# Performance work log

Measured on AMD Instinct MI355X. Metric: run time of the kernel, lower is better.

## Reference

```python
import jax, jax.numpy as jnp
import numpy as np

B, H, W, DIM = 16, 28, 28, 256
HEADS, K = 8, 7
HD = DIM // HEADS
MLP = int(DIM * 4.0)
EPS = 1e-5


def setup_inputs() -> dict:
    key = jax.random.key(0)
    ks = jax.random.split(key, 8)
    s = 0.02
    return {
        "x": jax.random.normal(ks[0], (B, H, W, DIM), jnp.float32),
        "norm1_w": jnp.ones((DIM,), jnp.float32),
        "norm1_b": jnp.zeros((DIM,), jnp.float32),
        "qkv_w": jax.random.normal(ks[1], (3 * DIM, DIM), jnp.float32) * s,
        "qkv_b": jnp.zeros((3 * DIM,), jnp.float32),
        "rpb": jax.random.normal(ks[2], (HEADS, 2 * K - 1, 2 * K - 1), jnp.float32) * s,
        "proj_w": jax.random.normal(ks[3], (DIM, DIM), jnp.float32) * s,
        "proj_b": jnp.zeros((DIM,), jnp.float32),
        "norm2_w": jnp.ones((DIM,), jnp.float32),
        "norm2_b": jnp.zeros((DIM,), jnp.float32),
        "fc1_w": jax.random.normal(ks[4], (MLP, DIM), jnp.float32) * s,
        "fc1_b": jnp.zeros((MLP,), jnp.float32),
        "fc2_w": jax.random.normal(ks[5], (DIM, MLP), jnp.float32) * s,
        "fc2_b": jnp.zeros((DIM,), jnp.float32),
    }


def _ln(x, w, b):
    m = jnp.mean(x, axis=-1, keepdims=True)
    v = jnp.var(x, axis=-1, keepdims=True)  # biased, as torch LayerNorm
    return (x - m) * jax.lax.rsqrt(v + EPS) * w + b


def _window_idx(n):
    # NATTEN border handling: window shifts so every query has exactly K neighbors
    start = jnp.clip(jnp.arange(n) - K // 2, 0, n - K)  # [n]
    idx = start[:, None] + jnp.arange(K)                # [n, K] absolute neighbor index
    rel = idx - jnp.arange(n)[:, None] + (K - 1)        # [n, K] rpb index in [0, 2K-2]
    return idx, rel


def _neighborhood_attn(x, qkv_w, qkv_b, rpb, proj_w, proj_b):
    b, h, w, c = x.shape
    qkv = (x @ qkv_w.T + qkv_b).reshape(b, h, w, 3, HEADS, HD)
    q, k, v = qkv[:, :, :, 0], qkv[:, :, :, 1], qkv[:, :, :, 2]  # [b,h,w,heads,hd]
    q = q * (HD ** -0.5)
    idx_h, rel_h = _window_idx(h)
    idx_w, rel_w = _window_idx(w)
    # gather K/V neighborhoods: [b,h,K,w,K,heads,hd]
    kwin = k[:, idx_h][:, :, :, idx_w]
    vwin = v[:, idx_h][:, :, :, idx_w]
    # logits per query (i,j) over its KxK window
    attn = jnp.einsum('bijhd,biajchd->bhijac', q, kwin)  # [b,heads,h,w,K,K]
    bias = rpb[:, rel_h]                 # [heads,h,K,2K-1]
    bias = bias[:, :, :, rel_w]          # [heads,h,K,w,K]
    bias = bias.transpose(0, 1, 3, 2, 4) # [heads,h,w,K,K]
    attn = attn + bias[None]
    attn = jax.nn.softmax(attn.reshape(b, HEADS, h, w, K * K), axis=-1)
    attn = attn.reshape(b, HEADS, h, w, K, K)
    out = jnp.einsum('bhijac,biajchd->bijhd', attn, vwin).reshape(b, h, w, c)
    return out @ proj_w.T + proj_b


def reference(x, norm1_w, norm1_b, qkv_w, qkv_b, rpb, proj_w, proj_b,
              norm2_w, norm2_b, fc1_w, fc1_b, fc2_w, fc2_b):
    shortcut = x
    x = _ln(x, norm1_w, norm1_b)
    x = shortcut + _neighborhood_attn(x, qkv_w, qkv_b, rpb, proj_w, proj_b)
    h = _ln(x, norm2_w, norm2_b) @ fc1_w.T + fc1_b
    h = jax.nn.gelu(h, approximate=False)  # torch nn.GELU default (erf)
    return x + (h @ fc2_w.T + fc2_b)
```

## Files before the change

kernel.cpp:

```cpp
#include <hip/hip_runtime.h>
#include <hip/hip_bf16.h>
#include <math.h>

#define DIM   256
#define HEADS 8
#define HD    32
#define KW    7
#define HH    28
#define WW    28
#define BBATCH 16
#define NTOK  (BBATCH*HH*WW)
#define MLPD  1024
#define EPSLN 1e-5f
#define QSCALE 0.17677669529663687f

#define AS1 __attribute__((address_space(1)))
#define AS3 __attribute__((address_space(3)))

typedef __attribute__((ext_vector_type(8))) short short8;
typedef __attribute__((ext_vector_type(4))) float f32x4;
typedef unsigned short us;

__device__ __forceinline__ float b2f(us u) {
  union { float f; unsigned u; } x; x.u = ((unsigned)u) << 16; return x.f;
}
__device__ __forceinline__ us f2b(float f) {
  union { float f; unsigned u; } x; x.f = f;
  unsigned lsb = (x.u >> 16) & 1;
  x.u += 0x7fffu + lsb;
  return (us)(x.u >> 16);
}
__device__ __forceinline__ bool probe_f32(const us* p) { return p[0] == 0; }

__device__ __forceinline__ void gll16(const us* g, us* l) {
  __builtin_amdgcn_global_load_lds((const AS1 unsigned*)(const void*)g,
                                   (AS3 unsigned*)(void*)l, 16, 0, 0);
}

__device__ __forceinline__ float gelu_f(float x) {
  const float y = 0.7978845608028654f * x * (1.0f + 0.044715f * x * x);
  const float u = __expf(2.0f * y);
  const float th = 1.0f - 2.0f / (u + 1.0f);
  return 0.5f * x * (1.0f + th);
}

__global__ __launch_bounds__(256) void pre_kernel(const void* s0, const void* s1,
                                                  const void* s2, const void* s3,
                                                  us* d0, us* d1, us* d2, us* d3,
                                                  const void* p0, const void* p1, const void* p2,
                                                  const void* p3, const void* p4, const void* p5,
                                                  const void* p6, const void* p7, const void* p8,
                                                  float* __restrict__ pack,
                                                  const void* __restrict__ x,
                                                  us* __restrict__ xn1,
                                                  us* __restrict__ bias_t,
                                                  const us* __restrict__ probe)
{
  const bool isf32 = probe_f32(probe);
  const int blk = blockIdx.x;
  const int t = threadIdx.x;
  if (blk < 768) {
    const int gi = (blk * 256 + t) * 4;
    const void* src; us* dst; int loc; bool qs = false;
    if (gi < 196608)      { src = s0; dst = d0; loc = gi; qs = (loc < 65536); }
    else if (gi < 262144) { src = s1; dst = d1; loc = gi - 196608; }
    else if (gi < 524288) { src = s2; dst = d2; loc = gi - 262144; }
    else                  { src = s3; dst = d3; loc = gi - 524288; }
    float v[4];
    if (isf32) {
      const float4 f = *(const float4*)((const float*)src + loc);
      v[0] = f.x; v[1] = f.y; v[2] = f.z; v[3] = f.w;
    } else {
      ushort4 u = *(const ushort4*)((const us*)src + loc);
      v[0] = b2f(u.x); v[1] = b2f(u.y); v[2] = b2f(u.z); v[3] = b2f(u.w);
    }
    const float sc = qs ? QSCALE : 1.0f;
    ushort4 o;
    o.x = f2b(v[0] * sc); o.y = f2b(v[1] * sc); o.z = f2b(v[2] * sc); o.w = f2b(v[3] * sc);
    *(ushort4*)(dst + loc) = o;
  } else if (blk < 777) {
    const int seg = blk - 768;
    const void* srcs[9] = {p0, p1, p2, p3, p4, p5, p6, p7, p8};
    const int offs[9] = {0, 256, 512, 1280, 1536, 1792, 2048, 3072, 3328};
    const int lens[9] = {256, 256, 768, 256, 256, 256, 1024, 256, 1352};
    const void* s = srcs[seg];
    const int off = offs[seg], len = lens[seg];
    for (int i = t; i < len; i += 256) {
      float v = isf32 ? ((const float*)s)[i] : b2f(((const us*)s)[i]);
      if (seg == 2 && i < 256) v *= QSCALE;
      pack[off + i] = v;
    }
  } else if (blk < 3913) {
    const int wave = t >> 6, lane = t & 63;
    const int tok = (blk - 777) * 4 + wave;
    const int c0 = lane * 4;
    float v[4];
    if (isf32) {
      const float4 f = *(const float4*)((const float*)x + (size_t)tok * DIM + c0);
      v[0] = f.x; v[1] = f.y; v[2] = f.z; v[3] = f.w;
    } else {
      ushort4 u = *(const ushort4*)((const us*)x + (size_t)tok * DIM + c0);
      v[0] = b2f(u.x); v[1] = b2f(u.y); v[2] = b2f(u.z); v[3] = b2f(u.w);
    }
    float s  = v[0] + v[1] + v[2] + v[3];
    float s2 = v[0]*v[0] + v[1]*v[1] + v[2]*v[2] + v[3]*v[3];
    #pragma unroll
    for (int m = 32; m; m >>= 1) { s += __shfl_xor(s, m); s2 += __shfl_xor(s2, m); }
    const float mean = s * (1.0f / DIM);
    const float var  = s2 * (1.0f / DIM) - mean * mean;
    const float rstd = rsqrtf(var + EPSLN);
    float wv[4], bv[4];
    if (isf32) {
      const float4 a = *(const float4*)((const float*)p0 + c0);
      const float4 c = *(const float4*)((const float*)p1 + c0);
      wv[0]=a.x; wv[1]=a.y; wv[2]=a.z; wv[3]=a.w;
      bv[0]=c.x; bv[1]=c.y; bv[2]=c.z; bv[3]=c.w;
    } else {
      ushort4 a = *(const ushort4*)((const us*)p0 + c0);
      ushort4 c = *(const ushort4*)((const us*)p1 + c0);
      wv[0]=b2f(a.x); wv[1]=b2f(a.y); wv[2]=b2f(a.z); wv[3]=b2f(a.w);
      bv[0]=b2f(c.x); bv[1]=b2f(c.y); bv[2]=b2f(c.z); bv[3]=b2f(c.w);
    }
    ushort4 o;
    o.x = f2b((v[0] - mean) * rstd * wv[0] + bv[0]);
    o.y = f2b((v[1] - mean) * rstd * wv[1] + bv[1]);
    o.z = f2b((v[2] - mean) * rstd * wv[2] + bv[2]);
    o.w = f2b((v[3] - mean) * rstd * wv[3] + bv[3]);
    *(ushort4*)(xn1 + (size_t)tok * DIM + c0) = o;
  } else {
    const int ph = blk - 3913;
    const int p  = ph >> 3, h = ph & 7;
    const int i0 = 2 * p;
    const int si0 = min(max(i0 - 3, 0), 21);
    us* bt = bias_t + (size_t)ph * (224 * 64);
    for (int e = 0; e < 56; ++e) {
      const int idx = e * 256 + t;
      const int kv = idx >> 6;
      const int q  = idx & 63;
      const int isub = q >> 5;
      const int cq = q & 31;
      const int iq = i0 + isub;
      const int siq = min(max(iq - 3, 0), 21);
      const int sj  = min(max(cq - 3, 0), 21);
      const int rr  = (kv * 2341) >> 16;
      const int ar  = si0 + rr;
      const int ck  = kv - rr * 28;
      const int dr = ar - siq, dc = ck - sj;
      const bool valid = (cq < 28) && (dr >= 0) && (dr < 7) && (dc >= 0) && (dc < 7);
      float ev = 0.f;
      if (valid) {
        const int ridx = h * 169 + (ar - iq + 6) * 13 + (ck - cq + 6);
        const float bvv = isf32 ? ((const float*)p8)[ridx] : b2f(((const us*)p8)[ridx]);
        ev = __expf(bvv);
      }
      bt[idx] = f2b(ev);
    }
  }
}

__global__ __launch_bounds__(256) void ln_kernel(const us* __restrict__ in,
                                                 const float* __restrict__ w,
                                                 const float* __restrict__ b,
                                                 us* __restrict__ out)
{
  const int t = threadIdx.x;
  const int wave = t >> 6, lane = t & 63;
  const int tok = blockIdx.x * 4 + wave;
  const int c0 = lane * 4;
  ushort4 u = *(const ushort4*)(in + (size_t)tok * DIM + c0);
  float v[4] = {b2f(u.x), b2f(u.y), b2f(u.z), b2f(u.w)};
  float s  = v[0] + v[1] + v[2] + v[3];
  float s2 = v[0]*v[0] + v[1]*v[1] + v[2]*v[2] + v[3]*v[3];
  #pragma unroll
  for (int m = 32; m; m >>= 1) { s += __shfl_xor(s, m); s2 += __shfl_xor(s2, m); }
  const float mean = s * (1.0f / DIM);
  const float var  = s2 * (1.0f / DIM) - mean * mean;
  const float rstd = rsqrtf(var + EPSLN);
  const float4 wv = *(const float4*)(w + c0);
  const float4 bv = *(const float4*)(b + c0);
  ushort4 o;
  o.x = f2b((v[0] - mean) * rstd * wv.x + bv.x);
  o.y = f2b((v[1] - mean) * rstd * wv.y + bv.y);
  o.z = f2b((v[2] - mean) * rstd * wv.z + bv.z);
  o.w = f2b((v[3] - mean) * rstd * wv.w + bv.w);
  *(ushort4*)(out + (size_t)tok * DIM + c0) = o;
}

template<int BM, int BN, int BK, int MODE>
__global__ __launch_bounds__(256) void gemm_kernel(const us* __restrict__ A,
                                                   const us* __restrict__ W,
                                                   const float* __restrict__ bias,
                                                   const void* __restrict__ resid,
                                                   void* __restrict__ out,
                                                   int N, int K,
                                                   const us* __restrict__ probe)
{
  constexpr int MF = BM / 32;
  constexpr int NF = BN / 32;
  constexpr int CPR = BK / 8;
  constexpr int ACH = BM * CPR;
  constexpr int BCH = BN * CPR;
  constexpr int ASZ = BM * BK;
  constexpr int BSZ = BN * BK;
  constexpr int TILEB = 2 * (ASZ + BSZ) * 2;
  constexpr int CSB = (MODE == 3) ? BM * BN * 4 : BM * BN * 2;
  constexpr int SMB = TILEB > CSB ? TILEB : CSB;
  __shared__ char smem[SMB];
  us* Asb = (us*)smem;
  us* Bsb = (us*)smem + 2 * ASZ;

  const int t = threadIdx.x;
  const int wave = t >> 6, lane = t & 63;
  const int wm = wave >> 1, wn = wave & 1;
  const int m0 = blockIdx.x * BM;
  const int n0 = blockIdx.y * BN;
  const int lm = lane & 15;
  const int g  = lane >> 4;

  const int NS = K / BK;

  #define STAGE(buf, kk)                                                         \
    {                                                                            \
      _Pragma("unroll")                                                          \
      for (int i = 0; i < ACH / 256; ++i) {                                      \
        const int slot = i * 256 + t;                                            \
        const int gc = slot ^ ((slot >> 3) & 7);                                 \
        gll16(A + (size_t)(m0 + gc / CPR) * K + (kk) + (gc % CPR) * 8,           \
              &Asb[(buf) * ASZ + slot * 8]);                                     \
      }                                                                          \
      _Pragma("unroll")                                                          \
      for (int i = 0; i < BCH / 256; ++i) {                                      \
        const int slot = i * 256 + t;                                            \
        const int gc = slot ^ ((slot >> 3) & 7);                                 \
        gll16(W + (size_t)(n0 + gc / CPR) * K + (kk) + (gc % CPR) * 8,           \
              &Bsb[(buf) * BSZ + slot * 8]);                                     \
      }                                                                          \
    }

  STAGE(0, 0);

  f32x4 acc[MF][NF] = {};
  int cur = 0;
  for (int s = 0; s < NS; ++s) {
    __syncthreads();
    if (s + 1 < NS) STAGE(cur ^ 1, (s + 1) * BK);
    #pragma unroll
    for (int kh = 0; kh < BK / 32; ++kh) {
      short8 a[MF], b[NF];
      #pragma unroll
      for (int mf = 0; mf < MF; ++mf) {
        const int row = wm * (BM / 2) + mf * 16 + lm;
        const int c = row * CPR + kh * 4 + g;
        const int sl = c ^ ((c >> 3) & 7);
        a[mf] = *(const short8*)(const void*)&Asb[cur * ASZ + sl * 8];
      }
      #pragma unroll
      for (int nf = 0; nf < NF; ++nf) {
        const int row = wn * (BN / 2) + nf * 16 + lm;
        const int c = row * CPR + kh * 4 + g;
        const int sl = c ^ ((c >> 3) & 7);
        b[nf] = *(const short8*)(const void*)&Bsb[cur * BSZ + sl * 8];
      }
      #pragma unroll
      for (int mf = 0; mf < MF; ++mf) {
        #pragma unroll
        for (int nf = 0; nf < NF; ++nf)
          acc[mf][nf] = __builtin_amdgcn_mfma_f32_16x16x32_bf16(a[mf], b[nf], acc[mf][nf], 0, 0, 0);
      }
    }
    cur ^= 1;
  }
  #undef STAGE

  const bool isf32 = (MODE == 1 || MODE == 3) ? probe_f32(probe) : false;
  const int col = lm;
  const int rb  = g * 4;
  __syncthreads();

  if (MODE == 3 && isf32) {
    float* Cf = (float*)smem;
    #pragma unroll
    for (int mf = 0; mf < MF; ++mf) {
      #pragma unroll
      for (int nf = 0; nf < NF; ++nf) {
        const int n_loc = wn * (BN / 2) + nf * 16 + col;
        const float bv = bias[n0 + n_loc];
        #pragma unroll
        for (int j = 0; j < 4; ++j) {
          const int m_loc = wm * (BM / 2) + mf * 16 + rb + j;
          const size_t off = (size_t)(m0 + m_loc) * N + (n0 + n_loc);
          float v = acc[mf][nf][j] + bv + b2f(((const us*)resid)[off]);
          Cf[m_loc * BN + (n_loc ^ ((m_loc & 7) << 3))] = v;
        }
      }
    }
    __syncthreads();
    constexpr int CH = BM * BN / 4;
    #pragma unroll
    for (int it = 0; it < CH / 256; ++it) {
      const int id = it * 256 + t;
      const int m = id / (BN / 4), c = id % (BN / 4);
      const float4 val = *(const float4*)&Cf[m * BN + ((c ^ ((m & 7) << 1)) * 4)];
      *(float4*)((float*)out + (size_t)(m0 + m) * N + n0 + c * 4) = val;
    }
  } else {
    us* Cs = (us*)smem;
    #pragma unroll
    for (int mf = 0; mf < MF; ++mf) {
      #pragma unroll
      for (int nf = 0; nf < NF; ++nf) {
        const int n_loc = wn * (BN / 2) + nf * 16 + col;
        const float bv = bias[n0 + n_loc];
        #pragma unroll
        for (int j = 0; j < 4; ++j) {
          const int m_loc = wm * (BM / 2) + mf * 16 + rb + j;
          const size_t off = (size_t)(m0 + m_loc) * N + (n0 + n_loc);
          float v = acc[mf][nf][j] + bv;
          if (MODE == 1) v += isf32 ? ((const float*)resid)[off] : b2f(((const us*)resid)[off]);
          else if (MODE == 2) v = gelu_f(v);
          else if (MODE == 3) v += b2f(((const us*)resid)[off]);
          Cs[m_loc * BN + (n_loc ^ ((m_loc & 7) << 3))] = f2b(v);
        }
      }
    }
    __syncthreads();
    constexpr int CH = BM * BN / 8;
    #pragma unroll
    for (int it = 0; it < CH / 256; ++it) {
      const int id = it * 256 + t;
      const int m = id / (BN / 8), c = id % (BN / 8);
      const uint4 val = *(const uint4*)&Cs[m * BN + (c ^ (m & 7)) * 8];
      *(uint4*)((us*)out + (size_t)(m0 + m) * N + n0 + c * 8) = val;
    }
  }
}

__global__ __launch_bounds__(256) void attn_kernel(const us* __restrict__ qkv,
                                                   const us* __restrict__ bias_t,
                                                   us* __restrict__ out)
{
  __shared__ us KP_lds[64 * 232];
  __shared__ us Vt_lds[32 * 232];

  const int raw = blockIdx.x;
  const int bid = (raw & 7) * 224 + (raw >> 3);
  const int b  = bid & 15;
  const int ph = bid >> 4;
  const int p  = ph >> 3;
  const int h  = ph & 7;
  const int i0 = 2 * p;
  const int t = threadIdx.x;
  const int wave = t >> 6, lane = t & 63;
  const int lm = lane & 15, g = lane >> 4;
  const int kb = g * 8;
  const int si0 = min(max(i0 - 3, 0), 21);
  const int si1 = min(max(i0 - 2, 0), 21);
  const int nch = (si1 + 7 - si0) * 112;

  const us* kg = qkv + ((size_t)(b * 784 + si0 * 28)) * 768 + 256 + h * 32;
  const us* vg = kg + 256;

  const int c0 = t, c1 = 256 + t, c2 = 512 + t, c3 = 768 + t;
  const bool has3 = c3 < nch;
  uint4 v0 = *(const uint4*)(const void*)(vg + (size_t)(c0 >> 2) * 768 + (c0 & 3) * 8);
  uint4 v1 = *(const uint4*)(const void*)(vg + (size_t)(c1 >> 2) * 768 + (c1 & 3) * 8);
  uint4 v2 = *(const uint4*)(const void*)(vg + (size_t)(c2 >> 2) * 768 + (c2 & 3) * 8);
  uint4 v3;
  if (has3) v3 = *(const uint4*)(const void*)(vg + (size_t)(c3 >> 2) * 768 + (c3 & 3) * 8);

  {
    int gk;
    gk = c0 ^ ((c0 >> 3) & 7); gll16(kg + (size_t)(gk >> 2) * 768 + (gk & 3) * 8, &KP_lds[c0 * 8]);
    gk = c1 ^ ((c1 >> 3) & 7); gll16(kg + (size_t)(gk >> 2) * 768 + (gk & 3) * 8, &KP_lds[c1 * 8]);
    gk = c2 ^ ((c2 >> 3) & 7); gll16(kg + (size_t)(gk >> 2) * 768 + (gk & 3) * 8, &KP_lds[c2 * 8]);
    if (has3) { gk = c3 ^ ((c3 >> 3) & 7); gll16(kg + (size_t)(gk >> 2) * 768 + (gk & 3) * 8, &KP_lds[c3 * 8]); }
  }

  if (nch == 784) {
    if (t < 112) *(uint4*)(void*)&KP_lds[(784 + t) * 8] = make_uint4(0, 0, 0, 0);
    const int ch = t & 31, slot = t >> 5;
    *(uint2*)(void*)&Vt_lds[ch * 232 + 196 + slot * 4] = make_uint2(0, 0);
  }

  {
    const unsigned uu0[4] = {v0.x, v0.y, v0.z, v0.w};
    const unsigned uu1[4] = {v1.x, v1.y, v1.z, v1.w};
    const unsigned uu2[4] = {v2.x, v2.y, v2.z, v2.w};
    #pragma unroll
    for (int e = 0; e < 4; ++e) {
      Vt_lds[((c0 & 3) * 8 + 2*e)     * 232 + (c0 >> 2)] = (us)(uu0[e] & 0xffffu);
      Vt_lds[((c0 & 3) * 8 + 2*e + 1) * 232 + (c0 >> 2)] = (us)(uu0[e] >> 16);
      Vt_lds[((c1 & 3) * 8 + 2*e)     * 232 + (c1 >> 2)] = (us)(uu1[e] & 0xffffu);
      Vt_lds[((c1 & 3) * 8 + 2*e + 1) * 232 + (c1 >> 2)] = (us)(uu1[e] >> 16);
      Vt_lds[((c2 & 3) * 8 + 2*e)     * 232 + (c2 >> 2)] = (us)(uu2[e] & 0xffffu);
      Vt_lds[((c2 & 3) * 8 + 2*e + 1) * 232 + (c2 >> 2)] = (us)(uu2[e] >> 16);
    }
    if (has3) {
      const unsigned uu3[4] = {v3.x, v3.y, v3.z, v3.w};
      #pragma unroll
      for (int e = 0; e < 4; ++e) {
        Vt_lds[((c3 & 3) * 8 + 2*e)     * 232 + (c3 >> 2)] = (us)(uu3[e] & 0xffffu);
        Vt_lds[((c3 & 3) * 8 + 2*e + 1) * 232 + (c3 >> 2)] = (us)(uu3[e] >> 16);
      }
    }
  }

  const int qcol_l = min((wave & 1) * 16 + lm, 27);
  const int iq = i0 + (wave >> 1);
  const short8 qa = *(const short8*)(const void*)(qkv + ((size_t)(b * 784 + iq * 28 + qcol_l)) * 768 + h * 32 + kb);

  __syncthreads();

  f32x4 s[14];
  #pragma unroll
  for (int n = 0; n < 14; ++n) {
    const int sl0 = (n * 16 + lm) * 4 + g;
    const int sl = sl0 ^ ((sl0 >> 3) & 7);
    const short8 kf = *(const short8*)(const void*)&KP_lds[sl * 8];
    f32x4 z = {0.f, 0.f, 0.f, 0.f};
    s[n] = __builtin_amdgcn_mfma_f32_16x16x32_bf16(qa, kf, z, 0, 0, 0);
  }

  __syncthreads();

  const us* bt = bias_t + (size_t)ph * (224 * 64);
  const int qb = wave * 16 + g * 4;
  float acc4[4] = {0.f, 0.f, 0.f, 0.f};
  #pragma unroll
  for (int n = 0; n < 14; ++n) {
    const ushort4 bb = *(const ushort4*)(const void*)&bt[(n * 16 + lm) * 64 + qb];
    const float eb[4] = {b2f(bb.x), b2f(bb.y), b2f(bb.z), b2f(bb.w)};
    #pragma unroll
    for (int jj = 0; jj < 4; ++jj) {
      const float e = __expf(s[n][jj]) * eb[jj];
      acc4[jj] += e;
      KP_lds[(qb + jj) * 232 + n * 16 + lm] = f2b(e);
    }
  }
  float sm[4];
  #pragma unroll
  for (int jj = 0; jj < 4; ++jj) {
    float v = acc4[jj];
    v += __shfl_xor(v, 1); v += __shfl_xor(v, 2);
    v += __shfl_xor(v, 4); v += __shfl_xor(v, 8);
    sm[jj] = v;
  }

  #pragma unroll
  for (int nto = 0; nto < 2; ++nto) {
    f32x4 o = {0.f, 0.f, 0.f, 0.f};
    #pragma unroll
    for (int ks = 0; ks < 7; ++ks) {
      const short8 pa = *(const short8*)(const void*)&KP_lds[(wave * 16 + lm) * 232 + ks * 32 + kb];
      const short8 vb = *(const short8*)(const void*)&Vt_lds[(nto * 16 + lm) * 232 + ks * 32 + kb];
      o = __builtin_amdgcn_mfma_f32_16x16x32_bf16(pa, vb, o, 0, 0, 0);
    }
    #pragma unroll
    for (int jj = 0; jj < 4; ++jj) {
      const int qc = (wave & 1) * 16 + g * 4 + jj;
      if (qc < 28) {
        const float inv = 1.0f / sm[jj];
        out[((size_t)(b * 784 + iq * 28 + qc)) * 256 + h * 32 + nto * 16 + lm] = f2b(o[jj] * inv);
      }
    }
  }
}

extern "C" void kernel_launch(void* const* d_in, const int* in_sizes, int n_in,
                              void* d_out, int out_size, void* d_ws, size_t ws_size,
                              hipStream_t stream)
{
  const us* probe = (const us*)d_in[1];

  char* ws = (char*)d_ws;
  us*    wqkv_c = (us*)(ws);
  us*    wproj_c= (us*)(ws + 393216);
  us*    wfc1_c = (us*)(ws + 524288);
  us*    wfc2_c = (us*)(ws + 1048576);
  float* pack   = (float*)(ws + 1572864);
  us*    bias_t = (us*)(ws + 1593344);
  us*    xn1    = (us*)(ws + 8015872);
  us*    qkv    = (us*)(ws + 14438400);
  us*    out1   = (us*)(ws + 33705984);
  us*    hbuf   = (us*)(ws + 40128512);
  us*    att    = xn1;
  us*    xn2    = qkv;

  const float* p_qkvb = pack + 512;
  const float* p_projb= pack + 1280;
  const float* p_n2w  = pack + 1536;
  const float* p_n2b  = pack + 1792;
  const float* p_fc1b = pack + 2048;
  const float* p_fc2b = pack + 3072;

  pre_kernel<<<4025, 256, 0, stream>>>(d_in[3], d_in[6], d_in[10], d_in[12],
                                       wqkv_c, wproj_c, wfc1_c, wfc2_c,
                                       d_in[1], d_in[2], d_in[4], d_in[7], d_in[8], d_in[9],
                                       d_in[11], d_in[13], d_in[5], pack,
                                       d_in[0], xn1, bias_t, probe);
  gemm_kernel<128, 128, 32, 0><<<dim3(NTOK / 128, 768 / 128), 256, 0, stream>>>(xn1, wqkv_c, p_qkvb, nullptr, qkv, 768, 256, probe);
  attn_kernel<<<BBATCH * (HH / 2) * HEADS, 256, 0, stream>>>(qkv, bias_t, att);
  gemm_kernel<64, 64, 64, 1><<<dim3(NTOK / 64, DIM / 64), 256, 0, stream>>>(att, wproj_c, p_projb, d_in[0], out1, DIM, 256, probe);
  ln_kernel<<<NTOK / 4, 256, 0, stream>>>(out1, p_n2w, p_n2b, xn2);
  gemm_kernel<128, 128, 32, 2><<<dim3(NTOK / 128, MLPD / 128), 256, 0, stream>>>(xn2, wfc1_c, p_fc1b, nullptr, hbuf, MLPD, 256, probe);
  gemm_kernel<64, 64, 64, 3><<<dim3(NTOK / 64, DIM / 64), 256, 0, stream>>>(hbuf, wfc2_c, p_fc2b, out1, d_out, DIM, MLPD, probe);
}
```

Before: 119.6 us.

## Split QKV GEMM output into Q, K and transposed V buffers for attention

```diff
diff --git a/kernel.cpp b/kernel.cpp
--- a/kernel.cpp
+++ b/kernel.cpp
@@ -192,6 +192,8 @@
                                                    const float* __restrict__ bias,
                                                    const void* __restrict__ resid,
                                                    void* __restrict__ out,
+                                                   void* __restrict__ out2,
+                                                   void* __restrict__ out3,
                                                    int N, int K,
                                                    const us* __restrict__ probe)
 {
@@ -277,7 +279,46 @@
   const int rb  = g * 4;
   __syncthreads();
 
-  if (MODE == 3 && isf32) {
+  if (MODE == 0) {
+    us* Cs = (us*)smem;
+    const bool isV = (n0 >= 512);
+    #pragma unroll
+    for (int mf = 0; mf < MF; ++mf) {
+      #pragma unroll
+      for (int nf = 0; nf < NF; ++nf) {
+        const int n_loc = wn * (BN / 2) + nf * 16 + col;
+        const float bv = bias[n0 + n_loc];
+        #pragma unroll
+        for (int j = 0; j < 4; ++j) {
+          const int m_loc = wm * (BM / 2) + mf * 16 + rb + j;
+          const us cv = f2b(acc[mf][nf][j] + bv);
+          if (isV) Cs[n_loc * BM + (m_loc ^ ((n_loc & 7) << 3))] = cv;
+          else     Cs[m_loc * BN + (n_loc ^ ((m_loc & 7) << 3))] = cv;
+        }
+      }
+    }
+    __syncthreads();
+    if (!isV) {
+      us* dst = (us*)(n0 < 256 ? out : out2);
+      const int nc0 = n0 & 255;
+      #pragma unroll
+      for (int it = 0; it < (BM * BN / 8) / 256; ++it) {
+        const int id = it * 256 + t;
+        const int m = id >> 4, c = id & 15;
+        const uint4 val = *(const uint4*)&Cs[m * BN + (c ^ (m & 7)) * 8];
+        *(uint4*)(dst + (size_t)(m0 + m) * 256 + nc0 + c * 8) = val;
+      }
+    } else {
+      us* dst = (us*)out3;
+      #pragma unroll
+      for (int it = 0; it < (BM * BN / 8) / 256; ++it) {
+        const int id = it * 256 + t;
+        const int n_loc = id >> 4, mc = id & 15;
+        const uint4 val = *(const uint4*)&Cs[n_loc * BM + (mc ^ (n_loc & 7)) * 8];
+        *(uint4*)(dst + (size_t)(n0 - 512 + n_loc) * NTOK + m0 + mc * 8) = val;
+      }
+    }
+  } else if (MODE == 3 && isf32) {
     float* Cf = (float*)smem;
     #pragma unroll
     for (int mf = 0; mf < MF; ++mf) {
@@ -295,9 +336,8 @@
       }
     }
     __syncthreads();
-    constexpr int CH = BM * BN / 4;
-    #pragma unroll
-    for (int it = 0; it < CH / 256; ++it) {
+    #pragma unroll
+    for (int it = 0; it < (BM * BN / 4) / 256; ++it) {
       const int id = it * 256 + t;
       const int m = id / (BN / 4), c = id % (BN / 4);
       const float4 val = *(const float4*)&Cf[m * BN + ((c ^ ((m & 7) << 1)) * 4)];
@@ -324,9 +364,8 @@
       }
     }
     __syncthreads();
-    constexpr int CH = BM * BN / 8;
-    #pragma unroll
-    for (int it = 0; it < CH / 256; ++it) {
+    #pragma unroll
+    for (int it = 0; it < (BM * BN / 8) / 256; ++it) {
       const int id = it * 256 + t;
       const int m = id / (BN / 8), c = id % (BN / 8);
       const uint4 val = *(const uint4*)&Cs[m * BN + (c ^ (m & 7)) * 8];
@@ -335,12 +374,14 @@
   }
 }
 
-__global__ __launch_bounds__(256) void attn_kernel(const us* __restrict__ qkv,
+__global__ __launch_bounds__(256) void attn_kernel(const us* __restrict__ q_buf,
+                                                   const us* __restrict__ kbuf,
+                                                   const us* __restrict__ vt,
                                                    const us* __restrict__ bias_t,
                                                    us* __restrict__ out)
 {
-  __shared__ us KP_lds[64 * 232];
-  __shared__ us Vt_lds[32 * 232];
+  __shared__ us KP[64 * 232];
+  __shared__ us Vt[32 * 256];
 
   const int raw = blockIdx.x;
   const int bid = (raw & 7) * 224 + (raw >> 3);
@@ -354,69 +395,40 @@
   const int lm = lane & 15, g = lane >> 4;
   const int kb = g * 8;
   const int si0 = min(max(i0 - 3, 0), 21);
-  const int si1 = min(max(i0 - 2, 0), 21);
-  const int nch = (si1 + 7 - si0) * 112;
-
-  const us* kg = qkv + ((size_t)(b * 784 + si0 * 28)) * 768 + 256 + h * 32;
-  const us* vg = kg + 256;
-
-  const int c0 = t, c1 = 256 + t, c2 = 512 + t, c3 = 768 + t;
-  const bool has3 = c3 < nch;
-  uint4 v0 = *(const uint4*)(const void*)(vg + (size_t)(c0 >> 2) * 768 + (c0 & 3) * 8);
-  uint4 v1 = *(const uint4*)(const void*)(vg + (size_t)(c1 >> 2) * 768 + (c1 & 3) * 8);
-  uint4 v2 = *(const uint4*)(const void*)(vg + (size_t)(c2 >> 2) * 768 + (c2 & 3) * 8);
-  uint4 v3;
-  if (has3) v3 = *(const uint4*)(const void*)(vg + (size_t)(c3 >> 2) * 768 + (c3 & 3) * 8);
-
-  {
-    int gk;
-    gk = c0 ^ ((c0 >> 3) & 7); gll16(kg + (size_t)(gk >> 2) * 768 + (gk & 3) * 8, &KP_lds[c0 * 8]);
-    gk = c1 ^ ((c1 >> 3) & 7); gll16(kg + (size_t)(gk >> 2) * 768 + (gk & 3) * 8, &KP_lds[c1 * 8]);
-    gk = c2 ^ ((c2 >> 3) & 7); gll16(kg + (size_t)(gk >> 2) * 768 + (gk & 3) * 8, &KP_lds[c2 * 8]);
-    if (has3) { gk = c3 ^ ((c3 >> 3) & 7); gll16(kg + (size_t)(gk >> 2) * 768 + (gk & 3) * 8, &KP_lds[c3 * 8]); }
-  }
-
-  if (nch == 784) {
-    if (t < 112) *(uint4*)(void*)&KP_lds[(784 + t) * 8] = make_uint4(0, 0, 0, 0);
-    const int ch = t & 31, slot = t >> 5;
-    *(uint2*)(void*)&Vt_lds[ch * 232 + 196 + slot * 4] = make_uint2(0, 0);
-  }
-
-  {
-    const unsigned uu0[4] = {v0.x, v0.y, v0.z, v0.w};
-    const unsigned uu1[4] = {v1.x, v1.y, v1.z, v1.w};
-    const unsigned uu2[4] = {v2.x, v2.y, v2.z, v2.w};
-    #pragma unroll
-    for (int e = 0; e < 4; ++e) {
-      Vt_lds[((c0 & 3) * 8 + 2*e)     * 232 + (c0 >> 2)] = (us)(uu0[e] & 0xffffu);
-      Vt_lds[((c0 & 3) * 8 + 2*e + 1) * 232 + (c0 >> 2)] = (us)(uu0[e] >> 16);
-      Vt_lds[((c1 & 3) * 8 + 2*e)     * 232 + (c1 >> 2)] = (us)(uu1[e] & 0xffffu);
-      Vt_lds[((c1 & 3) * 8 + 2*e + 1) * 232 + (c1 >> 2)] = (us)(uu1[e] >> 16);
-      Vt_lds[((c2 & 3) * 8 + 2*e)     * 232 + (c2 >> 2)] = (us)(uu2[e] & 0xffffu);
-      Vt_lds[((c2 & 3) * 8 + 2*e + 1) * 232 + (c2 >> 2)] = (us)(uu2[e] >> 16);
-    }
-    if (has3) {
-      const unsigned uu3[4] = {v3.x, v3.y, v3.z, v3.w};
-      #pragma unroll
-      for (int e = 0; e < 4; ++e) {
-        Vt_lds[((c3 & 3) * 8 + 2*e)     * 232 + (c3 >> 2)] = (us)(uu3[e] & 0xffffu);
-        Vt_lds[((c3 & 3) * 8 + 2*e + 1) * 232 + (c3 >> 2)] = (us)(uu3[e] >> 16);
-      }
-    }
+
+  const us* kgb = kbuf + (size_t)(b * 784 + si0 * 28) * 256 + h * 32;
+  #pragma unroll
+  for (int p4 = 0; p4 < 3; ++p4) {
+    const int s = p4 * 256 + t;
+    const int gk = s ^ ((s >> 3) & 7);
+    gll16(kgb + (size_t)(gk >> 2) * 256 + (gk & 3) * 8, &KP[s * 8]);
+  }
+  if (t < 128) {
+    const int s = 768 + t;
+    const int gk = s ^ ((s >> 3) & 7);
+    gll16(kgb + (size_t)(gk >> 2) * 256 + (gk & 3) * 8, &KP[s * 8]);
+  }
+  const us* vgb = vt + (size_t)(h * 32) * NTOK + b * 784 + si0 * 28;
+  #pragma unroll
+  for (int p4 = 0; p4 < 4; ++p4) {
+    const int s = p4 * 256 + t;
+    const int ch = s >> 5;
+    const int ck = (s ^ ((s >> 5) & 7)) & 31;
+    gll16(vgb + (size_t)ch * NTOK + ck * 8, &Vt[s * 8]);
   }
 
   const int qcol_l = min((wave & 1) * 16 + lm, 27);
   const int iq = i0 + (wave >> 1);
-  const short8 qa = *(const short8*)(const void*)(qkv + ((size_t)(b * 784 + iq * 28 + qcol_l)) * 768 + h * 32 + kb);
+  const short8 qa = *(const short8*)(const void*)(q_buf + (size_t)(b * 784 + iq * 28 + qcol_l) * 256 + h * 32 + kb);
 
   __syncthreads();
 
   f32x4 s[14];
   #pragma unroll
   for (int n = 0; n < 14; ++n) {
-    const int sl0 = (n * 16 + lm) * 4 + g;
-    const int sl = sl0 ^ ((sl0 >> 3) & 7);
-    const short8 kf = *(const short8*)(const void*)&KP_lds[sl * 8];
+    const int c = (n * 16 + lm) * 4 + g;
+    const int sl = c ^ ((c >> 3) & 7);
+    const short8 kf = *(const short8*)(const void*)&KP[sl * 8];
     f32x4 z = {0.f, 0.f, 0.f, 0.f};
     s[n] = __builtin_amdgcn_mfma_f32_16x16x32_bf16(qa, kf, z, 0, 0, 0);
   }
@@ -434,7 +446,7 @@
     for (int jj = 0; jj < 4; ++jj) {
       const float e = __expf(s[n][jj]) * eb[jj];
       acc4[jj] += e;
-      KP_lds[(qb + jj) * 232 + n * 16 + lm] = f2b(e);
+      KP[(qb + jj) * 232 + n * 16 + lm] = f2b(e);
     }
   }
   float sm[4];
@@ -449,10 +461,12 @@
   #pragma unroll
   for (int nto = 0; nto < 2; ++nto) {
     f32x4 o = {0.f, 0.f, 0.f, 0.f};
+    const int ch = nto * 16 + lm;
     #pragma unroll
     for (int ks = 0; ks < 7; ++ks) {
-      const short8 pa = *(const short8*)(const void*)&KP_lds[(wave * 16 + lm) * 232 + ks * 32 + kb];
-      const short8 vb = *(const short8*)(const void*)&Vt_lds[(nto * 16 + lm) * 232 + ks * 32 + kb];
+      const short8 pa = *(const short8*)(const void*)&KP[(wave * 16 + lm) * 232 + ks * 32 + kb];
+      const int c = ch * 32 + ks * 4 + g;
+      const short8 vb = *(const short8*)(const void*)&Vt[(c ^ (ch & 7)) * 8];
       o = __builtin_amdgcn_mfma_f32_16x16x32_bf16(pa, vb, o, 0, 0, 0);
     }
     #pragma unroll
@@ -460,7 +474,7 @@
       const int qc = (wave & 1) * 16 + g * 4 + jj;
       if (qc < 28) {
         const float inv = 1.0f / sm[jj];
-        out[((size_t)(b * 784 + iq * 28 + qc)) * 256 + h * 32 + nto * 16 + lm] = f2b(o[jj] * inv);
+        out[(size_t)(b * 784 + iq * 28 + qc) * 256 + h * 32 + nto * 16 + lm] = f2b(o[jj] * inv);
       }
     }
   }
@@ -479,12 +493,14 @@
   us*    wfc2_c = (us*)(ws + 1048576);
   float* pack   = (float*)(ws + 1572864);
   us*    bias_t = (us*)(ws + 1593344);
-  us*    xn1    = (us*)(ws + 8015872);
-  us*    qkv    = (us*)(ws + 14438400);
-  us*    out1   = (us*)(ws + 33705984);
-  us*    hbuf   = (us*)(ws + 40128512);
+  us*    xn1    = (us*)(ws + 4804608);
+  us*    q_buf  = (us*)(ws + 11227136);
+  us*    k_buf  = (us*)(ws + 17649664);
+  us*    vt     = (us*)(ws + 24088576);
+  us*    out1   = (us*)(ws + 30527488);
+  us*    hbuf   = (us*)(ws + 36950016);
   us*    att    = xn1;
-  us*    xn2    = qkv;
+  us*    xn2    = q_buf;
 
   const float* p_qkvb = pack + 512;
   const float* p_projb= pack + 1280;
@@ -498,10 +514,14 @@
                                        d_in[1], d_in[2], d_in[4], d_in[7], d_in[8], d_in[9],
                                        d_in[11], d_in[13], d_in[5], pack,
                                        d_in[0], xn1, bias_t, probe);
-  gemm_kernel<128, 128, 32, 0><<<dim3(NTOK / 128, 768 / 128), 256, 0, stream>>>(xn1, wqkv_c, p_qkvb, nullptr, qkv, 768, 256, probe);
-  attn_kernel<<<BBATCH * (HH / 2) * HEADS, 256, 0, stream>>>(qkv, bias_t, att);
-  gemm_kernel<64, 64, 64, 1><<<dim3(NTOK / 64, DIM / 64), 256, 0, stream>>>(att, wproj_c, p_projb, d_in[0], out1, DIM, 256, probe);
+  gemm_kernel<128, 128, 32, 0><<<dim3(NTOK / 128, 768 / 128), 256, 0, stream>>>(
+      xn1, wqkv_c, p_qkvb, nullptr, q_buf, k_buf, vt, 768, 256, probe);
+  attn_kernel<<<BBATCH * (HH / 2) * HEADS, 256, 0, stream>>>(q_buf, k_buf, vt, bias_t, att);
+  gemm_kernel<64, 64, 64, 1><<<dim3(NTOK / 64, DIM / 64), 256, 0, stream>>>(
+      att, wproj_c, p_projb, d_in[0], out1, nullptr, nullptr, DIM, 256, probe);
   ln_kernel<<<NTOK / 4, 256, 0, stream>>>(out1, p_n2w, p_n2b, xn2);
-  gemm_kernel<128, 128, 32, 2><<<dim3(NTOK / 128, MLPD / 128), 256, 0, stream>>>(xn2, wfc1_c, p_fc1b, nullptr, hbuf, MLPD, 256, probe);
-  gemm_kernel<64, 64, 64, 3><<<dim3(NTOK / 64, DIM / 64), 256, 0, stream>>>(hbuf, wfc2_c, p_fc2b, out1, d_out, DIM, MLPD, probe);
-}
+  gemm_kernel<128, 128, 32, 2><<<dim3(NTOK / 128, MLPD / 128), 256, 0, stream>>>(
+      xn2, wfc1_c, p_fc1b, nullptr, hbuf, nullptr, nullptr, MLPD, 256, probe);
+  gemm_kernel<64, 128, 64, 3><<<dim3(NTOK / 64, DIM / 128), 256, 0, stream>>>(
+      hbuf, wfc2_c, p_fc2b, out1, d_out, nullptr, nullptr, DIM, MLPD, probe);
+}
```

New measurement: 118.7 us. No clear change (-0.7%).
